# Kernel optimization log

Hardware: AMD Instinct MI355X
Metric: run time of the kernel (lower is better)

## Reference

```python
import jax, jax.numpy as jnp
import numpy as np


def setup_inputs() -> dict:
    key = jax.random.key(0)
    k1, k2, k3, k4 = jax.random.split(key, 4)
    B, C = 32768, 1000
    y_pred = jax.random.normal(k1, (B, C), dtype=jnp.float32)
    y_true = jax.random.randint(k2, (B,), 0, C, dtype=jnp.int64)
    distance_matrix = jax.random.uniform(k3, (C, C), dtype=jnp.float32)
    fix_layer = jax.random.normal(k4, (C, C), dtype=jnp.float32)
    return {"y_pred": y_pred, "y_true": y_true,
            "distance_matrix": distance_matrix, "fix_layer": fix_layer}


def reference(y_pred, y_true, distance_matrix, fix_layer):
    # log_softmax over classes
    logp = jax.nn.log_softmax(y_pred, axis=1)              # [B, C]
    pred = jnp.argmax(y_pred, axis=1)                      # [B]
    # h_matrix[i] = distance_matrix[pred_i, target_i] / max(distance_matrix)
    h = distance_matrix[pred, y_true] / jnp.max(distance_matrix)  # [B]
    # loss = -sum(log_softmax * one_hot(target) * h) / B
    # one_hot gather == logp[i, target_i]
    per_sample = logp[jnp.arange(y_pred.shape[0]), y_true] * h    # [B]
    # NOTE: fix_layer feeds h_weights in the original, which is dead code.
    loss = -jnp.sum(per_sample) / y_true.shape[0]
    return loss
```

## Files before the change

kernel.cpp:

```cpp
#include <hip/hip_runtime.h>
#include <math.h>

#define NCLASS 1000
#define NCHUNK 250
#define ROWS_PER_WAVE 4
#define WAVES_PER_BLOCK 4
#define ROWS_PER_BLOCK (ROWS_PER_WAVE * WAVES_PER_BLOCK)

__global__ __launch_bounds__(256) void hce_main(
    const float* __restrict__ y_pred,
    const int*   __restrict__ y_true,
    const float* __restrict__ D,
    float* __restrict__ partial,
    int nb, int dsize)
{
    const int tid  = threadIdx.x;
    const int lane = tid & 63;
    const int wave = tid >> 6;
    const int b    = blockIdx.x;

    float dm = -1.0f;
    for (int i = b * 256 + tid; i < dsize; i += nb * 256)
        dm = fmaxf(dm, D[i]);
    #pragma unroll
    for (int off = 32; off; off >>= 1)
        dm = fmaxf(dm, __shfl_xor(dm, off, 64));

    __shared__ float smax[WAVES_PER_BLOCK];
    __shared__ float ssum[WAVES_PER_BLOCK];
    if (lane == 0) smax[wave] = dm;

    float acc = 0.0f;
    const int row0 = b * ROWS_PER_BLOCK + wave * ROWS_PER_WAVE;
    for (int r = 0; r < ROWS_PER_WAVE; ++r) {
        const int row = row0 + r;
        const float4* rp4 = (const float4*)(y_pred + (size_t)row * NCLASS);

        float4 v[4];
        #pragma unroll
        for (int t = 0; t < 4; ++t) {
            int c = lane + 64 * t;
            if (c < NCHUNK) v[t] = rp4[c];
        }
        const int nt = (lane + 192 < NCHUNK) ? 4 : 3;

        float m = -INFINITY; int arg = 0;
        #pragma unroll
        for (int t = 0; t < 4; ++t) {
            if (t < nt) {
                int col = 4 * (lane + 64 * t);
                if (v[t].x > m) { m = v[t].x; arg = col;     }
                if (v[t].y > m) { m = v[t].y; arg = col + 1; }
                if (v[t].z > m) { m = v[t].z; arg = col + 2; }
                if (v[t].w > m) { m = v[t].w; arg = col + 3; }
            }
        }
        #pragma unroll
        for (int off = 32; off; off >>= 1) {
            float om = __shfl_xor(m,   off, 64);
            int   oa = __shfl_xor(arg, off, 64);
            if (om > m || (om == m && oa < arg)) { m = om; arg = oa; }
        }

        float s = 0.0f;
        #pragma unroll
        for (int t = 0; t < 4; ++t) {
            if (t < nt) {
                s += __expf(v[t].x - m) + __expf(v[t].y - m)
                   + __expf(v[t].z - m) + __expf(v[t].w - m);
            }
        }
        #pragma unroll
        for (int off = 32; off; off >>= 1)
            s += __shfl_xor(s, off, 64);

        if (lane == 0) {
            int   tgt  = y_true[row];
            float xt   = y_pred[(size_t)row * NCLASS + tgt];
            float logp = xt - m - __logf(s);
            float d    = D[arg * NCLASS + tgt];
            acc += logp * d;
        }
    }

    if (lane == 0) ssum[wave] = acc;
    __syncthreads();
    if (tid == 0) {
        partial[b]      = ssum[0] + ssum[1] + ssum[2] + ssum[3];
        partial[nb + b] = fmaxf(fmaxf(smax[0], smax[1]),
                                fmaxf(smax[2], smax[3]));
    }
}

__global__ __launch_bounds__(256) void hce_finalize(
    const float* __restrict__ partial, int nb,
    float* __restrict__ out, float invB)
{
    const int tid  = threadIdx.x;
    const int lane = tid & 63;
    const int wave = tid >> 6;
    float s = 0.0f, mx = -1.0f;
    for (int i = tid; i < nb; i += 256) {
        s  += partial[i];
        mx  = fmaxf(mx, partial[nb + i]);
    }
    #pragma unroll
    for (int off = 32; off; off >>= 1) {
        s  += __shfl_xor(s, off, 64);
        mx  = fmaxf(mx, __shfl_xor(mx, off, 64));
    }
    __shared__ float ss[4], sm[4];
    if (lane == 0) { ss[wave] = s; sm[wave] = mx; }
    __syncthreads();
    if (tid == 0) {
        float S = ss[0] + ss[1] + ss[2] + ss[3];
        float M = fmaxf(fmaxf(sm[0], sm[1]), fmaxf(sm[2], sm[3]));
        out[0] = -S * invB / M;
    }
}

extern "C" void kernel_launch(void* const* d_in, const int* in_sizes, int n_in,
                              void* d_out, int out_size, void* d_ws, size_t ws_size,
                              hipStream_t stream) {
    const float* y_pred = (const float*)d_in[0];
    const int*   y_true = (const int*)  d_in[1];
    const float* D      = (const float*)d_in[2];
    float* out = (float*)d_out;
    float* ws  = (float*)d_ws;

    const int B     = in_sizes[1];
    const int dsize = in_sizes[2];
    const int nb    = B / ROWS_PER_BLOCK;

    hce_main<<<nb, 256, 0, stream>>>(y_pred, y_true, D, ws, nb, dsize);
    hce_finalize<<<1, 256, 0, stream>>>(ws, nb, out, 1.0f / (float)B);
}
```

Before: 200.9 us.

## Batch all four rows' loads upfront and interleave per-row reductions

Loads of all four rows per wave are issued before any computation, together with the target indices and target logits spread across lanes 0-3. Each reduction step is then interleaved across the four rows to increase memory-level and instruction-level parallelism. The final D gather and log for each row run on separate lanes instead of serially on lane 0. This trades higher register use (with a min-blocks launch bound of 4) for fewer serialized memory round-trips per wave.

```diff
diff --git a/kernel.cpp b/kernel.cpp
--- a/kernel.cpp
+++ b/kernel.cpp
@@ -7,7 +7,7 @@
 #define WAVES_PER_BLOCK 4
 #define ROWS_PER_BLOCK (ROWS_PER_WAVE * WAVES_PER_BLOCK)
 
-__global__ __launch_bounds__(256) void hce_main(
+__global__ __launch_bounds__(256, 4) void hce_main(
     const float* __restrict__ y_pred,
     const int*   __restrict__ y_true,
     const float* __restrict__ D,
@@ -18,10 +18,29 @@
     const int lane = tid & 63;
     const int wave = tid >> 6;
     const int b    = blockIdx.x;
+    const int row0 = b * ROWS_PER_BLOCK + wave * ROWS_PER_WAVE;
+
+    int tgt = 0;
+    if (lane < ROWS_PER_WAVE) tgt = y_true[row0 + lane];
+
+    float4 v[ROWS_PER_WAVE][4];
+    #pragma unroll
+    for (int r = 0; r < ROWS_PER_WAVE; ++r) {
+        const float4* rp4 = (const float4*)(y_pred + (size_t)(row0 + r) * NCLASS);
+        #pragma unroll
+        for (int t = 0; t < 4; ++t) {
+            int c = lane + 64 * t;
+            if (c < NCHUNK) v[r][t] = rp4[c];
+        }
+    }
 
     float dm = -1.0f;
     for (int i = b * 256 + tid; i < dsize; i += nb * 256)
         dm = fmaxf(dm, D[i]);
+
+    float xt = 0.0f;
+    if (lane < ROWS_PER_WAVE) xt = y_pred[(size_t)(row0 + lane) * NCLASS + tgt];
+
     #pragma unroll
     for (int off = 32; off; off >>= 1)
         dm = fmaxf(dm, __shfl_xor(dm, off, 64));
@@ -30,58 +49,68 @@
     __shared__ float ssum[WAVES_PER_BLOCK];
     if (lane == 0) smax[wave] = dm;
 
-    float acc = 0.0f;
-    const int row0 = b * ROWS_PER_BLOCK + wave * ROWS_PER_WAVE;
+    const int nt = (lane + 192 < NCHUNK) ? 4 : 3;
+
+    float m[ROWS_PER_WAVE]; int arg[ROWS_PER_WAVE];
+    #pragma unroll
     for (int r = 0; r < ROWS_PER_WAVE; ++r) {
-        const int row = row0 + r;
-        const float4* rp4 = (const float4*)(y_pred + (size_t)row * NCLASS);
-
-        float4 v[4];
-        #pragma unroll
-        for (int t = 0; t < 4; ++t) {
-            int c = lane + 64 * t;
-            if (c < NCHUNK) v[t] = rp4[c];
-        }
-        const int nt = (lane + 192 < NCHUNK) ? 4 : 3;
-
-        float m = -INFINITY; int arg = 0;
+        m[r] = -INFINITY; arg[r] = 0;
         #pragma unroll
         for (int t = 0; t < 4; ++t) {
             if (t < nt) {
                 int col = 4 * (lane + 64 * t);
-                if (v[t].x > m) { m = v[t].x; arg = col;     }
-                if (v[t].y > m) { m = v[t].y; arg = col + 1; }
-                if (v[t].z > m) { m = v[t].z; arg = col + 2; }
-                if (v[t].w > m) { m = v[t].w; arg = col + 3; }
+                if (v[r][t].x > m[r]) { m[r] = v[r][t].x; arg[r] = col;     }
+                if (v[r][t].y > m[r]) { m[r] = v[r][t].y; arg[r] = col + 1; }
+                if (v[r][t].z > m[r]) { m[r] = v[r][t].z; arg[r] = col + 2; }
+                if (v[r][t].w > m[r]) { m[r] = v[r][t].w; arg[r] = col + 3; }
             }
         }
+    }
+    #pragma unroll
+    for (int off = 32; off; off >>= 1) {
         #pragma unroll
-        for (int off = 32; off; off >>= 1) {
-            float om = __shfl_xor(m,   off, 64);
-            int   oa = __shfl_xor(arg, off, 64);
-            if (om > m || (om == m && oa < arg)) { m = om; arg = oa; }
+        for (int r = 0; r < ROWS_PER_WAVE; ++r) {
+            float om = __shfl_xor(m[r],   off, 64);
+            int   oa = __shfl_xor(arg[r], off, 64);
+            if (om > m[r] || (om == m[r] && oa < arg[r])) { m[r] = om; arg[r] = oa; }
         }
+    }
 
-        float s = 0.0f;
+    float s[ROWS_PER_WAVE];
+    #pragma unroll
+    for (int r = 0; r < ROWS_PER_WAVE; ++r) {
+        s[r] = 0.0f;
         #pragma unroll
         for (int t = 0; t < 4; ++t) {
             if (t < nt) {
-                s += __expf(v[t].x - m) + __expf(v[t].y - m)
-                   + __expf(v[t].z - m) + __expf(v[t].w - m);
+                s[r] += __expf(v[r][t].x - m[r]) + __expf(v[r][t].y - m[r])
+                      + __expf(v[r][t].z - m[r]) + __expf(v[r][t].w - m[r]);
             }
         }
+    }
+    #pragma unroll
+    for (int off = 32; off; off >>= 1) {
         #pragma unroll
-        for (int off = 32; off; off >>= 1)
-            s += __shfl_xor(s, off, 64);
+        for (int r = 0; r < ROWS_PER_WAVE; ++r)
+            s[r] += __shfl_xor(s[r], off, 64);
+    }
 
-        if (lane == 0) {
-            int   tgt  = y_true[row];
-            float xt   = y_pred[(size_t)row * NCLASS + tgt];
-            float logp = xt - m - __logf(s);
-            float d    = D[arg * NCLASS + tgt];
-            acc += logp * d;
-        }
+    float mr = m[0], sr = s[0]; int ar = arg[0];
+    if (lane == 1) { mr = m[1]; sr = s[1]; ar = arg[1]; }
+    if (lane == 2) { mr = m[2]; sr = s[2]; ar = arg[2]; }
+    if (lane == 3) { mr = m[3]; sr = s[3]; ar = arg[3]; }
+
+    float contrib = 0.0f;
+    if (lane < ROWS_PER_WAVE) {
+        float d = D[(size_t)ar * NCLASS + tgt];
+        contrib = (xt - mr - __logf(sr)) * d;
     }
+
+    float c0 = __shfl(contrib, 0, 64);
+    float c1 = __shfl(contrib, 1, 64);
+    float c2 = __shfl(contrib, 2, 64);
+    float c3 = __shfl(contrib, 3, 64);
+    float acc = ((c0 + c1) + c2) + c3;
 
     if (lane == 0) ssum[wave] = acc;
     __syncthreads();
```

New measurement: 201.6 us. Within noise of the previous version (+0.4%).

## Assign one row per wave with 1024-thread blocks and issue loads early

Applied to the files above, without the earlier changes.

Restructures the main kernel so each of 16 waves in a 1024-thread block handles a single row, instead of each of 4 waves looping over 4 rows. The row loads, target index and target logit are issued before the distance-matrix max loop so their memory latency overlaps that loop. This raises the number of independent loads in flight per CU and drops the serial per-wave row loop. The cost is larger blocks with a launch-bounds hint that limits registers, plus a 16-way shared-memory reduction.

```diff
diff --git a/kernel.cpp b/kernel.cpp
--- a/kernel.cpp
+++ b/kernel.cpp
@@ -3,11 +3,11 @@
 
 #define NCLASS 1000
 #define NCHUNK 250
-#define ROWS_PER_WAVE 4
-#define WAVES_PER_BLOCK 4
-#define ROWS_PER_BLOCK (ROWS_PER_WAVE * WAVES_PER_BLOCK)
+#define WAVES_PER_BLOCK 16
+#define ROWS_PER_BLOCK 16
+#define BLOCK 1024
 
-__global__ __launch_bounds__(256) void hce_main(
+__global__ __launch_bounds__(1024, 8) void hce_main(
     const float* __restrict__ y_pred,
     const int*   __restrict__ y_true,
     const float* __restrict__ D,
@@ -18,9 +18,24 @@
     const int lane = tid & 63;
     const int wave = tid >> 6;
     const int b    = blockIdx.x;
+    const int row  = b * ROWS_PER_BLOCK + wave;
+
+    int tgt = 0;
+    if (lane == 0) tgt = y_true[row];
+
+    const float4* rp4 = (const float4*)(y_pred + (size_t)row * NCLASS);
+    float4 v[4];
+    #pragma unroll
+    for (int t = 0; t < 4; ++t) {
+        int c = lane + 64 * t;
+        if (c < NCHUNK) v[t] = rp4[c];
+    }
+
+    float xt = 0.0f;
+    if (lane == 0) xt = y_pred[(size_t)row * NCLASS + tgt];
 
     float dm = -1.0f;
-    for (int i = b * 256 + tid; i < dsize; i += nb * 256)
+    for (int i = b * BLOCK + tid; i < dsize; i += nb * BLOCK)
         dm = fmaxf(dm, D[i]);
     #pragma unroll
     for (int off = 32; off; off >>= 1)
@@ -30,65 +45,57 @@
     __shared__ float ssum[WAVES_PER_BLOCK];
     if (lane == 0) smax[wave] = dm;
 
-    float acc = 0.0f;
-    const int row0 = b * ROWS_PER_BLOCK + wave * ROWS_PER_WAVE;
-    for (int r = 0; r < ROWS_PER_WAVE; ++r) {
-        const int row = row0 + r;
-        const float4* rp4 = (const float4*)(y_pred + (size_t)row * NCLASS);
+    const int nt = (lane + 192 < NCHUNK) ? 4 : 3;
 
-        float4 v[4];
-        #pragma unroll
-        for (int t = 0; t < 4; ++t) {
-            int c = lane + 64 * t;
-            if (c < NCHUNK) v[t] = rp4[c];
-        }
-        const int nt = (lane + 192 < NCHUNK) ? 4 : 3;
-
-        float m = -INFINITY; int arg = 0;
-        #pragma unroll
-        for (int t = 0; t < 4; ++t) {
-            if (t < nt) {
-                int col = 4 * (lane + 64 * t);
-                if (v[t].x > m) { m = v[t].x; arg = col;     }
-                if (v[t].y > m) { m = v[t].y; arg = col + 1; }
-                if (v[t].z > m) { m = v[t].z; arg = col + 2; }
-                if (v[t].w > m) { m = v[t].w; arg = col + 3; }
-            }
-        }
-        #pragma unroll
-        for (int off = 32; off; off >>= 1) {
-            float om = __shfl_xor(m,   off, 64);
-            int   oa = __shfl_xor(arg, off, 64);
-            if (om > m || (om == m && oa < arg)) { m = om; arg = oa; }
-        }
-
-        float s = 0.0f;
-        #pragma unroll
-        for (int t = 0; t < 4; ++t) {
-            if (t < nt) {
-                s += __expf(v[t].x - m) + __expf(v[t].y - m)
-                   + __expf(v[t].z - m) + __expf(v[t].w - m);
-            }
-        }
-        #pragma unroll
-        for (int off = 32; off; off >>= 1)
-            s += __shfl_xor(s, off, 64);
-
-        if (lane == 0) {
-            int   tgt  = y_true[row];
-            float xt   = y_pred[(size_t)row * NCLASS + tgt];
-            float logp = xt - m - __logf(s);
-            float d    = D[arg * NCLASS + tgt];
-            acc += logp * d;
+    float m = -INFINITY; int arg = 0;
+    #pragma unroll
+    for (int t = 0; t < 4; ++t) {
+        if (t < nt) {
+            int col = 4 * (lane + 64 * t);
+            if (v[t].x > m) { m = v[t].x; arg = col;     }
+            if (v[t].y > m) { m = v[t].y; arg = col + 1; }
+            if (v[t].z > m) { m = v[t].z; arg = col + 2; }
+            if (v[t].w > m) { m = v[t].w; arg = col + 3; }
         }
     }
+    #pragma unroll
+    for (int off = 32; off; off >>= 1) {
+        float om = __shfl_xor(m,   off, 64);
+        int   oa = __shfl_xor(arg, off, 64);
+        if (om > m || (om == m && oa < arg)) { m = om; arg = oa; }
+    }
 
-    if (lane == 0) ssum[wave] = acc;
+    float s = 0.0f;
+    #pragma unroll
+    for (int t = 0; t < 4; ++t) {
+        if (t < nt) {
+            s += __expf(v[t].x - m) + __expf(v[t].y - m)
+               + __expf(v[t].z - m) + __expf(v[t].w - m);
+        }
+    }
+    #pragma unroll
+    for (int off = 32; off; off >>= 1)
+        s += __shfl_xor(s, off, 64);
+
+    if (lane == 0) {
+        float logp = xt - m - __logf(s);
+        float d    = D[(size_t)arg * NCLASS + tgt];
+        ssum[wave] = logp * d;
+    }
     __syncthreads();
+
     if (tid == 0) {
-        partial[b]      = ssum[0] + ssum[1] + ssum[2] + ssum[3];
-        partial[nb + b] = fmaxf(fmaxf(smax[0], smax[1]),
-                                fmaxf(smax[2], smax[3]));
+        float a0 = ((ssum[0]  + ssum[1])  + ssum[2])  + ssum[3];
+        float a1 = ((ssum[4]  + ssum[5])  + ssum[6])  + ssum[7];
+        float a2 = ((ssum[8]  + ssum[9])  + ssum[10]) + ssum[11];
+        float a3 = ((ssum[12] + ssum[13]) + ssum[14]) + ssum[15];
+        partial[b] = ((a0 + a1) + a2) + a3;
+
+        float m01 = fmaxf(fmaxf(smax[0],  smax[1]),  fmaxf(smax[2],  smax[3]));
+        float m23 = fmaxf(fmaxf(smax[4],  smax[5]),  fmaxf(smax[6],  smax[7]));
+        float m45 = fmaxf(fmaxf(smax[8],  smax[9]),  fmaxf(smax[10], smax[11]));
+        float m67 = fmaxf(fmaxf(smax[12], smax[13]), fmaxf(smax[14], smax[15]));
+        partial[nb + b] = fmaxf(fmaxf(m01, m23), fmaxf(m45, m67));
     }
 }
 
@@ -132,6 +139,6 @@
     const int dsize = in_sizes[2];
     const int nb    = B / ROWS_PER_BLOCK;
 
-    hce_main<<<nb, 256, 0, stream>>>(y_pred, y_true, D, ws, nb, dsize);
+    hce_main<<<nb, BLOCK, 0, stream>>>(y_pred, y_true, D, ws, nb, dsize);
     hce_finalize<<<1, 256, 0, stream>>>(ws, nb, out, 1.0f / (float)B);
 }
```

Result: faster. 195.6 us (-2.6%).
